# Kernel tuning notes

Hardware: AMD Instinct MI355X
Metric: run time of the kernel (lower is better)

## Reference

```python
import jax, jax.numpy as jnp
import numpy as np


def setup_inputs() -> dict:
    key = jax.random.key(0)
    k1, k2 = jax.random.split(key)
    B, H, W = 32, 512, 512
    H_SHAPE = (3, 3)  # filter shape -> w has h0*h1 - 1 = 8 taps
    x = jax.random.normal(k1, (B, H, W, 1), dtype=jnp.float32)
    w = jax.random.uniform(k2, (1, H_SHAPE[0] * H_SHAPE[1] - 1), dtype=jnp.float32)
    return {"x": x, "w": w}


def reference(x, w):
    # x: [B, H, W, 1] float32, w: [1, h0*h1-1] float32
    B, H, W = x.shape[0], x.shape[1], x.shape[2]
    xm = x.reshape(-1, H, W)  # [B, H, W]

    # Zero-pad the filter taps to the full [H, W] grid (top-left placement).
    hm1 = jnp.pad(w, ((0, H - w.shape[0]), (0, W - w.shape[1])))

    cplx = jnp.complex64
    # Inverse filter spectrum and its three flipped/rolled (frequency-reversed) copies.
    gm1f = 1.0 / jnp.fft.fft2(hm1.astype(cplx))                 # [H, W]
    gm2f = jnp.roll(jnp.flip(gm1f, axis=0), shift=1, axis=0)
    gm3f = jnp.roll(jnp.flip(gm1f, axis=1), shift=1, axis=1)
    gm4f = jnp.roll(jnp.flip(gm3f, axis=0), shift=1, axis=0)
    gmf = (gm1f * gm2f) * (gm3f * gm4f)                         # [H, W]

    # Apply combined inverse filter in the frequency domain.
    ymf = gmf * jnp.fft.fft2(xm.astype(cplx))                   # [B, H, W]
    ym = jnp.real(jnp.fft.ifft2(ymf)).astype(jnp.float32)       # tf.cast complex->float takes real part
    return ym.reshape(-1, H, W, 1)
```

## Files before the change

### kernel.cpp

```cpp
#include <hip/hip_runtime.h>


#define WDIM 512
#define PAIRS_PER_BLOCK 4

struct cplx { float re, im; };
__device__ __forceinline__ cplx cadd(cplx a, cplx b) { return {a.re + b.re, a.im + b.im}; }
__device__ __forceinline__ cplx csub(cplx a, cplx b) { return {a.re - b.re, a.im - b.im}; }
__device__ __forceinline__ cplx cmul(cplx a, cplx b) {
    return {a.re * b.re - a.im * b.im, a.re * b.im + a.im * b.re};
}
template <int SIGN> __device__ __forceinline__ cplx cmul_i(cplx a) {
    return (SIGN > 0) ? cplx{-a.im, a.re} : cplx{a.im, -a.re};
}

template <int SIGN> __device__ __forceinline__ cplx wroot512(int k) {
    float f = (float)k * (1.0f / 512.0f);
    float sn = __builtin_amdgcn_sinf(f);
    float cs = __builtin_amdgcn_cosf(f);
    return {cs, SIGN > 0 ? sn : -sn};
}

template <int SIGN> __device__ __forceinline__ void dft8(const cplx* a, cplx* b) {
    cplx t0 = cadd(a[0], a[4]), t4 = csub(a[0], a[4]);
    cplx t1 = cadd(a[1], a[5]), t5 = csub(a[1], a[5]);
    cplx t2 = cadd(a[2], a[6]), t6 = cmul_i<SIGN>(csub(a[2], a[6]));
    cplx t3 = cadd(a[3], a[7]), t7 = cmul_i<SIGN>(csub(a[3], a[7]));
    cplx E0 = cadd(t0, t2), E2 = csub(t0, t2);
    cplx E1 = cadd(t4, t6), E3 = csub(t4, t6);
    cplx O0 = cadd(t1, t3), O2 = csub(t1, t3);
    cplx O1 = cadd(t5, t7), O3 = csub(t5, t7);
    const float C = 0.70710678118654752f;
    cplx w1 = {C, SIGN * C};
    cplx w3 = {-C, SIGN * C};
    cplx O1w = cmul(O1, w1);
    cplx O2w = cmul_i<SIGN>(O2);
    cplx O3w = cmul(O3, w3);
    b[0] = cadd(E0, O0);  b[4] = csub(E0, O0);
    b[1] = cadd(E1, O1w); b[5] = csub(E1, O1w);
    b[2] = cadd(E2, O2w); b[6] = csub(E2, O2w);
    b[3] = cadd(E3, O3w); b[7] = csub(E3, O3w);
}

template <int SIGN> __device__ __forceinline__ void twiddle8(cplx* b, int k512) {
#pragma unroll
    for (int t = 1; t < 8; ++t) {
        cplx w = wroot512<SIGN>((k512 * t) & 511);
        b[t] = cmul(b[t], w);
    }
}

__device__ __forceinline__ int phi(int q) { return q + ((q >> 6) << 2); }

__global__ __launch_bounds__(256, 4) void fft_conv_kernel(const float* __restrict__ x,
                                                          const float* __restrict__ w,
                                                          float* __restrict__ y) {
    __shared__ float lds[PAIRS_PER_BLOCK][2][544];
    const int wv = threadIdx.x >> 6;
    const int u = threadIdx.x & 63;
    const int pair = blockIdx.x * PAIRS_PER_BLOCK + wv;
    float* lre = lds[wv][0];
    float* lim = lds[wv][1];
    const float* x1 = x + (size_t)(2 * pair) * WDIM;
    const float* x2 = x1 + WDIM;

    cplx a[8], b[8];
#pragma unroll
    for (int j = 0; j < 8; ++j) {
        int idx = u + 64 * j;
        a[j].re = x1[idx];
        a[j].im = x2[idx];
    }

    float Gv[8];
    {
        const int c = ((u & 7) << 3) + (u >> 3);
        cplx m[8], Hv[8];
        m[0] = {w[0], 0.0f};
#pragma unroll
        for (int j = 1; j < 8; ++j) {
            cplx e = wroot512<-1>((c * j) & 511);
            float wj = w[j];
            m[j].re = wj * e.re;
            m[j].im = wj * e.im;
        }
        dft8<-1>(m, Hv);
#pragma unroll
        for (int t = 0; t < 8; ++t) {
            float m2 = Hv[t].re * Hv[t].re + Hv[t].im * Hv[t].im;
            Gv[t] = 1.0f / (m2 * m2);
        }
    }

    dft8<-1>(a, b);
    twiddle8<-1>(b, u);
#pragma unroll
    for (int t = 0; t < 8; ++t) {
        int p = phi(u + 64 * t);
        lre[p] = b[t].re; lim[p] = b[t].im;
    }
    __syncthreads();

    {
        const int base = ((u >> 3) << 6) + (u & 7);
#pragma unroll
        for (int j = 0; j < 8; ++j) {
            int p = phi(base + 8 * j);
            a[j].re = lre[p]; a[j].im = lim[p];
        }
        dft8<-1>(a, b);
        twiddle8<-1>(b, 8 * (u & 7));
#pragma unroll
        for (int t = 0; t < 8; ++t) {
            int p = phi(base + 8 * t);
            lre[p] = b[t].re; lim[p] = b[t].im;
        }
    }
    __syncthreads();

    {
        const int base = 8 * u;
#pragma unroll
        for (int j = 0; j < 8; ++j) {
            int p = phi(base + j);
            a[j].re = lre[p]; a[j].im = lim[p];
        }
        dft8<-1>(a, b);
#pragma unroll
        for (int t = 0; t < 8; ++t) {
            b[t].re *= Gv[t]; b[t].im *= Gv[t];
        }
        dft8<+1>(b, a);
#pragma unroll
        for (int j = 0; j < 8; ++j) {
            int p = phi(base + j);
            lre[p] = a[j].re; lim[p] = a[j].im;
        }
    }
    __syncthreads();

    {
        const int base = ((u >> 3) << 6) + (u & 7);
#pragma unroll
        for (int t = 0; t < 8; ++t) {
            int p = phi(base + 8 * t);
            a[t].re = lre[p]; a[t].im = lim[p];
        }
        twiddle8<+1>(a, 8 * (u & 7));
        dft8<+1>(a, b);
#pragma unroll
        for (int j = 0; j < 8; ++j) {
            int p = phi(base + 8 * j);
            lre[p] = b[j].re; lim[p] = b[j].im;
        }
    }
    __syncthreads();

    {
#pragma unroll
        for (int t = 0; t < 8; ++t) {
            int p = phi(u + 64 * t);
            a[t].re = lre[p]; a[t].im = lim[p];
        }
        twiddle8<+1>(a, u);
        dft8<+1>(a, b);
        const float s = 1.0f / 512.0f;
        float* y1 = y + (size_t)(2 * pair) * WDIM;
        float* y2 = y1 + WDIM;
#pragma unroll
        for (int j = 0; j < 8; ++j) {
            int idx = u + 64 * j;
            y1[idx] = b[j].re * s;
            y2[idx] = b[j].im * s;
        }
    }
}

extern "C" void kernel_launch(void* const* d_in, const int* in_sizes, int n_in,
                              void* d_out, int out_size, void* d_ws, size_t ws_size,
                              hipStream_t stream) {
    const float* x = (const float*)d_in[0];
    const float* w = (const float*)d_in[1];
    float* y = (float*)d_out;

    fft_conv_kernel<<<dim3(16384 / (2 * PAIRS_PER_BLOCK)), dim3(256), 0, stream>>>(x, w, y);
}
```

Baseline: 88.36 us.

## Use one-wave blocks, precomputed twiddles, float2 LDS and folded scaling

Each block now runs a single 64-thread wave on one row pair instead of four waves sharing a block. The per-thread twiddle sines and cosines are computed once up front and reused by the matching forward and inverse passes instead of being recomputed. LDS becomes one interleaved float2 array with a smaller padding stride, the filter-spectrum computation moves after two FFT passes, and the 1/512 output scale is folded into Gv. The aim is fewer transcendental instructions, less LDS traffic and lighter barriers, at the cost of extra registers for the cached twiddles and more, smaller blocks.

```diff
diff --git a/kernel.cpp b/kernel.cpp
--- a/kernel.cpp
+++ b/kernel.cpp
@@ -2,7 +2,6 @@
 
 
 #define WDIM 512
-#define PAIRS_PER_BLOCK 4
 
 struct cplx { float re, im; };
 __device__ __forceinline__ cplx cadd(cplx a, cplx b) { return {a.re + b.re, a.im + b.im}; }
@@ -13,12 +12,8 @@
 template <int SIGN> __device__ __forceinline__ cplx cmul_i(cplx a) {
     return (SIGN > 0) ? cplx{-a.im, a.re} : cplx{a.im, -a.re};
 }
-
-template <int SIGN> __device__ __forceinline__ cplx wroot512(int k) {
-    float f = (float)k * (1.0f / 512.0f);
-    float sn = __builtin_amdgcn_sinf(f);
-    float cs = __builtin_amdgcn_cosf(f);
-    return {cs, SIGN > 0 ? sn : -sn};
+__device__ __forceinline__ cplx twmul(cplx v, float c, float s) {
+    return {v.re * c - v.im * s, v.im * c + v.re * s};
 }
 
 template <int SIGN> __device__ __forceinline__ void dft8(const cplx* a, cplx* b) {
@@ -42,137 +37,122 @@
     b[3] = cadd(E3, O3w); b[7] = csub(E3, O3w);
 }
 
-template <int SIGN> __device__ __forceinline__ void twiddle8(cplx* b, int k512) {
-#pragma unroll
-    for (int t = 1; t < 8; ++t) {
-        cplx w = wroot512<SIGN>((k512 * t) & 511);
-        b[t] = cmul(b[t], w);
-    }
-}
+__device__ __forceinline__ int phi(int q) { return q + ((q >> 6) << 1); }
 
-__device__ __forceinline__ int phi(int q) { return q + ((q >> 6) << 2); }
-
-__global__ __launch_bounds__(256, 4) void fft_conv_kernel(const float* __restrict__ x,
-                                                          const float* __restrict__ w,
-                                                          float* __restrict__ y) {
-    __shared__ float lds[PAIRS_PER_BLOCK][2][544];
-    const int wv = threadIdx.x >> 6;
-    const int u = threadIdx.x & 63;
-    const int pair = blockIdx.x * PAIRS_PER_BLOCK + wv;
-    float* lre = lds[wv][0];
-    float* lim = lds[wv][1];
+__global__ __launch_bounds__(64, 4) void fft_conv_kernel(const float* __restrict__ x,
+                                                         const float* __restrict__ w,
+                                                         float* __restrict__ y) {
+    __shared__ float2 l[528];
+    const int u = threadIdx.x;
+    const int pair = blockIdx.x;
     const float* x1 = x + (size_t)(2 * pair) * WDIM;
     const float* x2 = x1 + WDIM;
 
     cplx a[8], b[8];
 #pragma unroll
     for (int j = 0; j < 8; ++j) {
-        int idx = u + 64 * j;
-        a[j].re = x1[idx];
-        a[j].im = x2[idx];
+        int i = u + 64 * j;
+        a[j].re = x1[i];
+        a[j].im = x2[i];
     }
+
+    float c512[7], s512[7], c64[7], s64[7];
+#pragma unroll
+    for (int t = 1; t < 8; ++t) {
+        float f = (float)(u * t) * (1.0f / 512.0f);
+        s512[t - 1] = __builtin_amdgcn_sinf(f);
+        c512[t - 1] = __builtin_amdgcn_cosf(f);
+        float g = (float)((u & 7) * t) * (1.0f / 64.0f);
+        s64[t - 1] = __builtin_amdgcn_sinf(g);
+        c64[t - 1] = __builtin_amdgcn_cosf(g);
+    }
+
+    const int base = ((u >> 3) << 6) | (u & 7);
+
+    dft8<-1>(a, b);
+#pragma unroll
+    for (int t = 1; t < 8; ++t) b[t] = twmul(b[t], c512[t - 1], -s512[t - 1]);
+#pragma unroll
+    for (int t = 0; t < 8; ++t) l[phi(u + 64 * t)] = make_float2(b[t].re, b[t].im);
+    __syncthreads();
+
+#pragma unroll
+    for (int j = 0; j < 8; ++j) {
+        float2 v = l[phi(base + 8 * j)];
+        a[j].re = v.x; a[j].im = v.y;
+    }
+    dft8<-1>(a, b);
+#pragma unroll
+    for (int t = 1; t < 8; ++t) b[t] = twmul(b[t], c64[t - 1], -s64[t - 1]);
+#pragma unroll
+    for (int t = 0; t < 8; ++t) l[phi(base + 8 * t)] = make_float2(b[t].re, b[t].im);
+    __syncthreads();
 
     float Gv[8];
     {
-        const int c = ((u & 7) << 3) + (u >> 3);
+        const int c = ((u & 7) << 3) | (u >> 3);
         cplx m[8], Hv[8];
-        m[0] = {w[0], 0.0f};
+        m[0].re = w[0]; m[0].im = 0.0f;
 #pragma unroll
         for (int j = 1; j < 8; ++j) {
-            cplx e = wroot512<-1>((c * j) & 511);
+            float f = (float)(c * j) * (1.0f / 512.0f);
+            float sn = __builtin_amdgcn_sinf(f);
+            float cs = __builtin_amdgcn_cosf(f);
             float wj = w[j];
-            m[j].re = wj * e.re;
-            m[j].im = wj * e.im;
+            m[j].re = wj * cs;
+            m[j].im = -wj * sn;
         }
         dft8<-1>(m, Hv);
 #pragma unroll
         for (int t = 0; t < 8; ++t) {
             float m2 = Hv[t].re * Hv[t].re + Hv[t].im * Hv[t].im;
-            Gv[t] = 1.0f / (m2 * m2);
+            Gv[t] = (1.0f / 512.0f) / (m2 * m2);
         }
     }
 
-    dft8<-1>(a, b);
-    twiddle8<-1>(b, u);
+    {
+        const int cb = 8 * u;
 #pragma unroll
-    for (int t = 0; t < 8; ++t) {
-        int p = phi(u + 64 * t);
-        lre[p] = b[t].re; lim[p] = b[t].im;
+        for (int j = 0; j < 8; ++j) {
+            float2 v = l[phi(cb + j)];
+            a[j].re = v.x; a[j].im = v.y;
+        }
+        dft8<-1>(a, b);
+#pragma unroll
+        for (int t = 0; t < 8; ++t) { b[t].re *= Gv[t]; b[t].im *= Gv[t]; }
+        dft8<+1>(b, a);
+#pragma unroll
+        for (int j = 0; j < 8; ++j) l[phi(cb + j)] = make_float2(a[j].re, a[j].im);
     }
     __syncthreads();
 
-    {
-        const int base = ((u >> 3) << 6) + (u & 7);
 #pragma unroll
-        for (int j = 0; j < 8; ++j) {
-            int p = phi(base + 8 * j);
-            a[j].re = lre[p]; a[j].im = lim[p];
-        }
-        dft8<-1>(a, b);
-        twiddle8<-1>(b, 8 * (u & 7));
+    for (int t = 0; t < 8; ++t) {
+        float2 v = l[phi(base + 8 * t)];
+        a[t].re = v.x; a[t].im = v.y;
+    }
 #pragma unroll
-        for (int t = 0; t < 8; ++t) {
-            int p = phi(base + 8 * t);
-            lre[p] = b[t].re; lim[p] = b[t].im;
-        }
-    }
+    for (int t = 1; t < 8; ++t) a[t] = twmul(a[t], c64[t - 1], s64[t - 1]);
+    dft8<+1>(a, b);
+#pragma unroll
+    for (int j = 0; j < 8; ++j) l[phi(base + 8 * j)] = make_float2(b[j].re, b[j].im);
     __syncthreads();
 
-    {
-        const int base = 8 * u;
 #pragma unroll
-        for (int j = 0; j < 8; ++j) {
-            int p = phi(base + j);
-            a[j].re = lre[p]; a[j].im = lim[p];
-        }
-        dft8<-1>(a, b);
+    for (int t = 0; t < 8; ++t) {
+        float2 v = l[phi(u + 64 * t)];
+        a[t].re = v.x; a[t].im = v.y;
+    }
 #pragma unroll
-        for (int t = 0; t < 8; ++t) {
-            b[t].re *= Gv[t]; b[t].im *= Gv[t];
-        }
-        dft8<+1>(b, a);
+    for (int t = 1; t < 8; ++t) a[t] = twmul(a[t], c512[t - 1], s512[t - 1]);
+    dft8<+1>(a, b);
+    float* y1 = y + (size_t)(2 * pair) * WDIM;
+    float* y2 = y1 + WDIM;
 #pragma unroll
-        for (int j = 0; j < 8; ++j) {
-            int p = phi(base + j);
-            lre[p] = a[j].re; lim[p] = a[j].im;
-        }
-    }
-    __syncthreads();
-
-    {
-        const int base = ((u >> 3) << 6) + (u & 7);
-#pragma unroll
-        for (int t = 0; t < 8; ++t) {
-            int p = phi(base + 8 * t);
-            a[t].re = lre[p]; a[t].im = lim[p];
-        }
-        twiddle8<+1>(a, 8 * (u & 7));
-        dft8<+1>(a, b);
-#pragma unroll
-        for (int j = 0; j < 8; ++j) {
-            int p = phi(base + 8 * j);
-            lre[p] = b[j].re; lim[p] = b[j].im;
-        }
-    }
-    __syncthreads();
-
-    {
-#pragma unroll
-        for (int t = 0; t < 8; ++t) {
-            int p = phi(u + 64 * t);
-            a[t].re = lre[p]; a[t].im = lim[p];
-        }
-        twiddle8<+1>(a, u);
-        dft8<+1>(a, b);
-        const float s = 1.0f / 512.0f;
-        float* y1 = y + (size_t)(2 * pair) * WDIM;
-        float* y2 = y1 + WDIM;
-#pragma unroll
-        for (int j = 0; j < 8; ++j) {
-            int idx = u + 64 * j;
-            y1[idx] = b[j].re * s;
-            y2[idx] = b[j].im * s;
-        }
+    for (int j = 0; j < 8; ++j) {
+        int i = u + 64 * j;
+        y1[i] = b[j].re;
+        y2[i] = b[j].im;
     }
 }
 
@@ -183,5 +163,5 @@
     const float* w = (const float*)d_in[1];
     float* y = (float*)d_out;
 
-    fft_conv_kernel<<<dim3(16384 / (2 * PAIRS_PER_BLOCK)), dim3(256), 0, stream>>>(x, w, y);
+    fft_conv_kernel<<<dim3(8192), dim3(64), 0, stream>>>(x, w, y);
 }
```

Measured after the change: 86.92 us. About the same (-1.6%).
